# Optimization experiments

Hardware: AMD Instinct MI355X
Metric: run time of the kernel (lower is better)

## Reference

```python
import jax, jax.numpy as jnp
import numpy as np
import math

B = 512          # graphs per batch
NP = 200         # nodes per graph
E_PER = 2000     # edges per graph
V = 50000        # item vocab
EMB = 9
HID = 128
RATIO = 0.8
K1 = math.ceil(RATIO * NP)   # 160
K2 = math.ceil(RATIO * K1)   # 128
K3 = math.ceil(RATIO * K2)   # 103


def sage_conv(x, src, dst, valid, n, w_neigh, w_root, b):
    # PyG SAGEConv: lin_l(mean_{j->i} x_j) + lin_r(x_i) + bias
    msg = x[src] * valid[:, None]                      # [E, C]
    seg = jnp.where(valid > 0, dst, n)                 # invalid edges -> dummy segment
    s = jax.ops.segment_sum(msg, seg, num_segments=n + 1)[:n]
    cnt = jax.ops.segment_sum(valid, seg, num_segments=n + 1)[:n]
    mean = s / jnp.maximum(cnt, 1.0)[:, None]
    return mean @ w_neigh.T + x @ w_root.T + b


def topk_pool(x, src, dst, valid, np_cur, k, p):
    # TopKPooling: score = tanh(x.p/||p||); keep top-k per graph; x *= score
    n = x.shape[0]
    score = jnp.tanh((x @ p) / jnp.linalg.norm(p))
    topv, topi = jax.lax.top_k(score.reshape(B, np_cur), k)   # [B, k]
    kept = (jnp.arange(B)[:, None] * np_cur + topi).reshape(-1)
    n_new = B * k
    x_new = x[kept] * topv.reshape(-1)[:, None]
    mapping = jnp.full((n,), -1, dtype=jnp.int32).at[kept].set(
        jnp.arange(n_new, dtype=jnp.int32))
    ns, nd = mapping[src], mapping[dst]
    valid_new = valid * ((ns >= 0) & (nd >= 0)).astype(valid.dtype)
    return x_new, jnp.maximum(ns, 0), jnp.maximum(nd, 0), valid_new


def global_pool(x, k):
    # cat([global_max_pool, global_mean_pool]) with uniform graph size k
    xr = x.reshape(B, k, -1)
    return jnp.concatenate([xr.max(axis=1), xr.mean(axis=1)], axis=1)


def setup_inputs() -> dict:
    key = jax.random.key(0)
    ks = jax.random.split(key, 24)
    # block-structured intra-graph edges
    s = jax.random.randint(ks[0], (B, E_PER), 0, NP)
    d = jax.random.randint(ks[1], (B, E_PER), 0, NP)
    off = (jnp.arange(B) * NP)[:, None]
    edge_index = jnp.stack([(s + off).reshape(-1), (d + off).reshape(-1)]).astype(jnp.int32)
    node_ids = jax.random.randint(ks[2], (B * NP, 1), 0, V)
    batch = jnp.repeat(jnp.arange(B), NP)
    sc = 0.1
    p = {
        'emb': jax.random.normal(ks[3], (V, EMB)) * sc,
        'w1n': jax.random.normal(ks[4], (HID, EMB)) * sc,
        'w1r': jax.random.normal(ks[5], (HID, EMB)) * sc,
        'b1': jnp.zeros((HID,)),
        'w2n': jax.random.normal(ks[6], (HID, HID)) * sc,
        'w2r': jax.random.normal(ks[7], (HID, HID)) * sc,
        'b2': jnp.zeros((HID,)),
        'w3n': jax.random.normal(ks[8], (HID, HID)) * sc,
        'w3r': jax.random.normal(ks[9], (HID, HID)) * sc,
        'b3': jnp.zeros((HID,)),
        'p1': jax.random.normal(ks[10], (HID,)) * sc,
        'p2': jax.random.normal(ks[11], (HID,)) * sc,
        'p3': jax.random.normal(ks[12], (HID,)) * sc,
        'lw1': jax.random.normal(ks[13], (HID, 2 * HID)) * sc,
        'lb1': jnp.zeros((HID,)),
        'lw2': jax.random.normal(ks[14], (64, HID)) * sc,
        'lb2': jnp.zeros((64,)),
        'lw3': jax.random.normal(ks[15], (1, 64)) * sc,
        'lb3': jnp.zeros((1,)),
    }
    return {'node_ids': node_ids, 'edge_index': edge_index, 'batch': batch, **p}


def reference(node_ids, edge_index, batch, emb, w1n, w1r, b1, w2n, w2r, b2,
              w3n, w3r, b3, p1, p2, p3, lw1, lb1, lw2, lb2, lw3, lb3):
    src, dst = edge_index[0], edge_index[1]
    valid = jnp.ones(src.shape[0], dtype=jnp.float32)
    x = emb[node_ids[:, 0]]                                  # [N, 9]
    x = jax.nn.relu(sage_conv(x, src, dst, valid, B * NP, w1n, w1r, b1))
    x, src, dst, valid = topk_pool(x, src, dst, valid, NP, K1, p1)
    x1 = global_pool(x, K1)
    x = jax.nn.relu(sage_conv(x, src, dst, valid, B * K1, w2n, w2r, b2))
    x, src, dst, valid = topk_pool(x, src, dst, valid, K1, K2, p2)
    x2 = global_pool(x, K2)
    x = jax.nn.relu(sage_conv(x, src, dst, valid, B * K2, w3n, w3r, b3))
    x, src, dst, valid = topk_pool(x, src, dst, valid, K2, K3, p3)
    x3 = global_pool(x, K3)
    h = x1 + x2 + x3                                         # [B, 256]
    h = jax.nn.relu(h @ lw1.T + lb1)
    h = jax.nn.relu(h @ lw2.T + lb2)
    return jax.nn.sigmoid(h @ lw3.T + lb3)[:, 0]             # [B]
```

## Files before the change

### kernel.cpp

```cpp
#include <hip/hip_runtime.h>
#include <math.h>

constexpr int B    = 512;
constexpr int NPG  = 200;
constexpr int EPER = 2000;
constexpr int EMB  = 9;
constexpr int HID  = 128;
constexpr int K1   = 160;
constexpr int K2   = 128;
constexpr int K3   = 103;
constexpr int E    = B * EPER;

__global__ __launch_bounds__(640, 2) void k_fused(
        const int* __restrict__ node_ids,
        const float* __restrict__ emb,
        const int* __restrict__ es, const int* __restrict__ ed,
        const float* __restrict__ w1n, const float* __restrict__ w1r,
        const float* __restrict__ b1, const float* __restrict__ p1,
        const float* __restrict__ w2n, const float* __restrict__ w2r,
        const float* __restrict__ b2, const float* __restrict__ p2,
        const float* __restrict__ w3n, const float* __restrict__ w3r,
        const float* __restrict__ b3, const float* __restrict__ p3,
        float* __restrict__ g1, float* __restrict__ g2,
        float* __restrict__ g3) {
    const int g = blockIdx.x, tid = threadIdx.x;
    const int lane = tid & 63, wv = tid >> 6;

    __shared__ float xY[K1 * 132];
    __shared__ float S[2 * 32 * 132];
    __shared__ int   csr[EPER];
    __shared__ int   deg[256], scanb[256], off2[257], cur[256];
    __shared__ int   idsL[NPG];
    __shared__ float sc[NPG];
    __shared__ int   pos1[NPG], pos2[K1];

    const int eb = g * EPER, nb0 = g * NPG;

    {
        float* x0L  = S;
        float* mnL  = S + 1800;
        float* redA = S + 3600;
        if (tid < NPG) idsL[tid] = node_ids[g * NPG + tid];
        if (tid < 256) deg[tid] = 0;
        __syncthreads();
        for (int i = tid; i < NPG * EMB; i += 640) {
            int n = i / EMB, j = i - n * EMB;
            x0L[i] = emb[(size_t)idsL[n] * EMB + j];
        }
        for (int e = tid; e < EPER; e += 640)
            atomicAdd(&deg[ed[eb + e] - nb0], 1);
        __syncthreads();
        if (tid < 256) scanb[tid] = deg[tid];
        __syncthreads();
        #pragma unroll
        for (int d = 1; d < 256; d <<= 1) {
            int t = (tid < 256 && tid >= d) ? scanb[tid - d] : 0;
            __syncthreads();
            if (tid < 256) scanb[tid] += t;
            __syncthreads();
        }
        if (tid == 0) off2[0] = 0;
        if (tid < 256) off2[tid + 1] = scanb[tid];
        __syncthreads();
        if (tid < 256) cur[tid] = off2[tid];
        __syncthreads();
        for (int e = tid; e < EPER; e += 640) {
            int slot = atomicAdd(&cur[ed[eb + e] - nb0], 1);
            csr[slot] = es[eb + e] - nb0;
        }
        __syncthreads();
        if (tid < NPG) {
            int bg = off2[tid], en = off2[tid + 1];
            float a[EMB];
            #pragma unroll
            for (int j = 0; j < EMB; j++) a[j] = 0.f;
            for (int t = bg; t < en; t++) {
                int s = csr[t];
                #pragma unroll
                for (int j = 0; j < EMB; j++) a[j] += x0L[s * EMB + j];
            }
            float inv = 1.f / (float)((en - bg) > 1 ? (en - bg) : 1);
            #pragma unroll
            for (int j = 0; j < EMB; j++) mnL[tid * EMB + j] = a[j] * inv;
        }
        float pl0 = p1[lane], pl1 = p1[64 + lane];
        float pp = pl0 * pl0 + pl1 * pl1;
        #pragma unroll
        for (int o = 32; o >= 1; o >>= 1) pp += __shfl_xor(pp, o, 64);
        float nrm = sqrtf(pp);
        float wn0[EMB], wn1[EMB], wr0[EMB], wr1[EMB];
        #pragma unroll
        for (int j = 0; j < EMB; j++) {
            wn0[j] = w1n[lane * EMB + j];
            wn1[j] = w1n[(lane + 64) * EMB + j];
            wr0[j] = w1r[lane * EMB + j];
            wr1[j] = w1r[(lane + 64) * EMB + j];
        }
        float bb0 = b1[lane], bb1 = b1[64 + lane];
        __syncthreads();
        for (int i = wv; i < NPG; i += 10) {
            float c0 = bb0, c1 = bb1;
            #pragma unroll
            for (int j = 0; j < EMB; j++) {
                float m = mnL[i * EMB + j];
                float x = x0L[i * EMB + j];
                c0 += m * wn0[j] + x * wr0[j];
                c1 += m * wn1[j] + x * wr1[j];
            }
            c0 = fmaxf(c0, 0.f);
            c1 = fmaxf(c1, 0.f);
            float d = c0 * pl0 + c1 * pl1;
            #pragma unroll
            for (int o = 32; o >= 1; o >>= 1) d += __shfl_xor(d, o, 64);
            if (lane == 0) sc[i] = tanhf(d / nrm);
        }
        __syncthreads();
        if (tid < NPG) {
            float scv = sc[tid];
            int rank = 0;
            for (int j = 0; j < NPG; j++) {
                float o = sc[j];
                rank += (o > scv) || (o == scv && j < tid);
            }
            pos1[tid] = (rank < K1) ? rank : -1;
        }
        __syncthreads();
        float pm0 = -INFINITY, pm1 = -INFINITY, ps0 = 0.f, ps1 = 0.f;
        for (int i = wv; i < NPG; i += 10) {
            int r = pos1[i];
            if (r < 0) continue;
            float c0 = bb0, c1 = bb1;
            #pragma unroll
            for (int j = 0; j < EMB; j++) {
                float m = mnL[i * EMB + j];
                float x = x0L[i * EMB + j];
                c0 += m * wn0[j] + x * wr0[j];
                c1 += m * wn1[j] + x * wr1[j];
            }
            float s = sc[i];
            float v0 = fmaxf(c0, 0.f) * s;
            float v1 = fmaxf(c1, 0.f) * s;
            xY[r * 132 + lane] = v0;
            xY[r * 132 + 64 + lane] = v1;
            pm0 = fmaxf(pm0, v0); ps0 += v0;
            pm1 = fmaxf(pm1, v1); ps1 += v1;
        }
        redA[wv * 128 + lane] = pm0;
        redA[wv * 128 + 64 + lane] = pm1;
        redA[1280 + wv * 128 + lane] = ps0;
        redA[1280 + wv * 128 + 64 + lane] = ps1;
        __syncthreads();
        if (tid < 128) {
            float mx = redA[tid], sm = redA[1280 + tid];
            #pragma unroll
            for (int w = 1; w < 10; w++) {
                mx = fmaxf(mx, redA[w * 128 + tid]);
                sm += redA[1280 + w * 128 + tid];
            }
            g1[g * 256 + tid] = mx;
            g1[g * 256 + 128 + tid] = sm / (float)K1;
        }
        __syncthreads();
    }

    {
        if (tid < 256) deg[tid] = 0;
        __syncthreads();
        for (int e = tid; e < EPER; e += 640) {
            int a = pos1[es[eb + e] - nb0];
            int b = pos1[ed[eb + e] - nb0];
            if (a >= 0 && b >= 0) atomicAdd(&deg[b], 1);
        }
        __syncthreads();
        if (tid < 256) scanb[tid] = deg[tid];
        __syncthreads();
        #pragma unroll
        for (int d = 1; d < 256; d <<= 1) {
            int t = (tid < 256 && tid >= d) ? scanb[tid - d] : 0;
            __syncthreads();
            if (tid < 256) scanb[tid] += t;
            __syncthreads();
        }
        if (tid == 0) off2[0] = 0;
        if (tid < 256) off2[tid + 1] = scanb[tid];
        __syncthreads();
        if (tid < 256) cur[tid] = off2[tid];
        __syncthreads();
        for (int e = tid; e < EPER; e += 640) {
            int a = pos1[es[eb + e] - nb0];
            int b = pos1[ed[eb + e] - nb0];
            if (a >= 0 && b >= 0) {
                int slot = atomicAdd(&cur[b], 1);
                csr[slot] = a;
            }
        }
        __syncthreads();

        const int tc = tid & 31, tr = tid >> 5;
        float accY[8][4], accZ[8][4];
        #pragma unroll
        for (int r = 0; r < 8; r++)
            #pragma unroll
            for (int c = 0; c < 4; c++) { accY[r][c] = 0.f; accZ[r][c] = 0.f; }

        const int sr = tid >> 3, sc4 = (tid & 7) * 4;
        const bool stager = (sr < 64);
        const float* wsrc0 = (sr < 32) ? w2n : w2r;
        const int wrow = (sr < 32) ? sr : sr - 32;
        float* Bmine = S + ((sr < 32) ? 0 : 32 * 132);
        float4 bvv[4];
        if (stager) {
            #pragma unroll
            for (int i = 0; i < 4; i++)
                bvv[i] = *(const float4*)(wsrc0 + (size_t)(wrow + i * 32) * HID + sc4);
        }
        for (int ch = 0; ch < 4; ch++) {
            if (stager) {
                #pragma unroll
                for (int i = 0; i < 4; i++) {
                    int r = wrow + i * 32;
                    Bmine[(sc4 + 0) * 132 + r] = bvv[i].x;
                    Bmine[(sc4 + 1) * 132 + r] = bvv[i].y;
                    Bmine[(sc4 + 2) * 132 + r] = bvv[i].z;
                    Bmine[(sc4 + 3) * 132 + r] = bvv[i].w;
                }
            }
            __syncthreads();
            if (ch + 1 < 4 && stager) {
                #pragma unroll
                for (int i = 0; i < 4; i++)
                    bvv[i] = *(const float4*)(wsrc0 + (size_t)(wrow + i * 32) * HID
                                              + (ch + 1) * 32 + sc4);
            }
            for (int kq = 0; kq < 8; kq++) {
                float4 af[8];
                #pragma unroll
                for (int rr = 0; rr < 8; rr++)
                    af[rr] = *(const float4*)&xY[(tr * 8 + rr) * 132 + ch * 32 + kq * 4];
                #pragma unroll
                for (int kk = 0; kk < 4; kk++) {
                    int k = kq * 4 + kk;
                    float4 bn = *(const float4*)&S[k * 132 + tc * 4];
                    float4 br = *(const float4*)&S[32 * 132 + k * 132 + tc * 4];
                    #pragma unroll
                    for (int rr = 0; rr < 8; rr++) {
                        float a = (kk == 0) ? af[rr].x : (kk == 1) ? af[rr].y
                                 : (kk == 2) ? af[rr].z : af[rr].w;
                        accY[rr][0] += a * bn.x; accY[rr][1] += a * bn.y;
                        accY[rr][2] += a * bn.z; accY[rr][3] += a * bn.w;
                        accZ[rr][0] += a * br.x; accZ[rr][1] += a * br.y;
                        accZ[rr][2] += a * br.z; accZ[rr][3] += a * br.w;
                    }
                }
            }
            __syncthreads();
        }
        #pragma unroll
        for (int rr = 0; rr < 8; rr++) {
            float4 yv = {accY[rr][0], accY[rr][1], accY[rr][2], accY[rr][3]};
            *(float4*)&xY[(tr * 8 + rr) * 132 + tc * 4] = yv;
        }
        __syncthreads();

        float bias[4], pv[4];
        #pragma unroll
        for (int c = 0; c < 4; c++) {
            bias[c] = b2[tc * 4 + c];
            pv[c]   = p2[tc * 4 + c];
        }
        float a0 = p2[lane], a1 = p2[64 + lane];
        float pp = a0 * a0 + a1 * a1;
        #pragma unroll
        for (int o = 32; o >= 1; o >>= 1) pp += __shfl_xor(pp, o, 64);
        float nrm = sqrtf(pp);
        float outv[8][4];
        #pragma unroll
        for (int rr = 0; rr < 8; rr++) {
            int m = tr * 8 + rr;
            int bg = off2[m], en = off2[m + 1];
            float s0 = 0.f, s1 = 0.f, s2 = 0.f, s3 = 0.f;
            for (int t = bg; t < en; t++) {
                float4 yv = *(const float4*)&xY[csr[t] * 132 + tc * 4];
                s0 += yv.x; s1 += yv.y; s2 += yv.z; s3 += yv.w;
            }
            float inv = 1.f / (float)((en - bg) > 1 ? (en - bg) : 1);
            outv[rr][0] = fmaxf(s0 * inv + accZ[rr][0] + bias[0], 0.f);
            outv[rr][1] = fmaxf(s1 * inv + accZ[rr][1] + bias[1], 0.f);
            outv[rr][2] = fmaxf(s2 * inv + accZ[rr][2] + bias[2], 0.f);
            outv[rr][3] = fmaxf(s3 * inv + accZ[rr][3] + bias[3], 0.f);
        }
        float* scpart = S;
        __syncthreads();
        #pragma unroll
        for (int rr = 0; rr < 8; rr++) {
            float sp = outv[rr][0] * pv[0] + outv[rr][1] * pv[1]
                     + outv[rr][2] * pv[2] + outv[rr][3] * pv[3];
            scpart[(tr * 8 + rr) * 32 + tc] = sp;
        }
        __syncthreads();
        if (tid < K1) {
            float sum = 0.f;
            #pragma unroll
            for (int t = 0; t < 32; t++) sum += scpart[tid * 32 + t];
            sc[tid] = tanhf(sum / nrm);
        }
        __syncthreads();
        if (tid < K1) {
            float scv = sc[tid];
            int rank = 0;
            for (int j = 0; j < K1; j++) {
                float o = sc[j];
                rank += (o > scv) || (o == scv && j < tid);
            }
            pos2[tid] = (rank < K2) ? rank : -1;
        }
        __syncthreads();
        float cm[4], cs[4];
        #pragma unroll
        for (int c = 0; c < 4; c++) { cm[c] = -INFINITY; cs[c] = 0.f; }
        #pragma unroll
        for (int rr = 0; rr < 8; rr++) {
            int m = tr * 8 + rr;
            int r = pos2[m];
            if (r < 0) continue;
            float sv = sc[m];
            float v0 = outv[rr][0] * sv, v1 = outv[rr][1] * sv;
            float v2 = outv[rr][2] * sv, v3 = outv[rr][3] * sv;
            cm[0] = fmaxf(cm[0], v0); cs[0] += v0;
            cm[1] = fmaxf(cm[1], v1); cs[1] += v1;
            cm[2] = fmaxf(cm[2], v2); cs[2] += v2;
            cm[3] = fmaxf(cm[3], v3); cs[3] += v3;
            float4 o0 = {v0, v1, v2, v3};
            *(float4*)&xY[r * 132 + tc * 4] = o0;
        }
        float* redM = S;
        float* redS = S + 20 * 128;
        #pragma unroll
        for (int c = 0; c < 4; c++) {
            redM[tr * 128 + tc * 4 + c] = cm[c];
            redS[tr * 128 + tc * 4 + c] = cs[c];
        }
        __syncthreads();
        if (tid < 128) {
            float mx = redM[tid], sm = redS[tid];
            #pragma unroll 4
            for (int t = 1; t < 20; t++) {
                mx = fmaxf(mx, redM[t * 128 + tid]);
                sm += redS[t * 128 + tid];
            }
            g2[g * 256 + tid] = mx;
            g2[g * 256 + 128 + tid] = sm / (float)K2;
        }
        __syncthreads();
    }

    {
        if (tid < 256) deg[tid] = 0;
        __syncthreads();
        for (int e = tid; e < EPER; e += 640) {
            int a = pos1[es[eb + e] - nb0];
            int b = pos1[ed[eb + e] - nb0];
            a = (a >= 0) ? pos2[a] : -1;
            b = (b >= 0) ? pos2[b] : -1;
            if (a >= 0 && b >= 0) atomicAdd(&deg[b], 1);
        }
        __syncthreads();
        if (tid < 256) scanb[tid] = deg[tid];
        __syncthreads();
        #pragma unroll
        for (int d = 1; d < 256; d <<= 1) {
            int t = (tid < 256 && tid >= d) ? scanb[tid - d] : 0;
            __syncthreads();
            if (tid < 256) scanb[tid] += t;
            __syncthreads();
        }
        if (tid == 0) off2[0] = 0;
        if (tid < 256) off2[tid + 1] = scanb[tid];
        __syncthreads();
        if (tid < 256) cur[tid] = off2[tid];
        __syncthreads();
        for (int e = tid; e < EPER; e += 640) {
            int a = pos1[es[eb + e] - nb0];
            int b = pos1[ed[eb + e] - nb0];
            a = (a >= 0) ? pos2[a] : -1;
            b = (b >= 0) ? pos2[b] : -1;
            if (a >= 0 && b >= 0) {
                int slot = atomicAdd(&cur[b], 1);
                csr[slot] = a;
            }
        }
        __syncthreads();

        const int tc = tid & 31, tr = tid >> 5;
        const bool comp = (tid < 512);
        float accY[8][4], accZ[8][4];
        #pragma unroll
        for (int r = 0; r < 8; r++)
            #pragma unroll
            for (int c = 0; c < 4; c++) { accY[r][c] = 0.f; accZ[r][c] = 0.f; }

        const int sr = tid >> 3, sc4 = (tid & 7) * 4;
        const bool stager = (sr < 64);
        const float* wsrc0 = (sr < 32) ? w3n : w3r;
        const int wrow = (sr < 32) ? sr : sr - 32;
        float* Bmine = S + ((sr < 32) ? 0 : 32 * 132);
        float4 bvv[4];
        if (stager) {
            #pragma unroll
            for (int i = 0; i < 4; i++)
                bvv[i] = *(const float4*)(wsrc0 + (size_t)(wrow + i * 32) * HID + sc4);
        }
        for (int ch = 0; ch < 4; ch++) {
            if (stager) {
                #pragma unroll
                for (int i = 0; i < 4; i++) {
                    int r = wrow + i * 32;
                    Bmine[(sc4 + 0) * 132 + r] = bvv[i].x;
                    Bmine[(sc4 + 1) * 132 + r] = bvv[i].y;
                    Bmine[(sc4 + 2) * 132 + r] = bvv[i].z;
                    Bmine[(sc4 + 3) * 132 + r] = bvv[i].w;
                }
            }
            __syncthreads();
            if (ch + 1 < 4 && stager) {
                #pragma unroll
                for (int i = 0; i < 4; i++)
                    bvv[i] = *(const float4*)(wsrc0 + (size_t)(wrow + i * 32) * HID
                                              + (ch + 1) * 32 + sc4);
            }
            if (comp) {
                for (int kq = 0; kq < 8; kq++) {
                    float4 af[8];
                    #pragma unroll
                    for (int rr = 0; rr < 8; rr++)
                        af[rr] = *(const float4*)&xY[(tr * 8 + rr) * 132 + ch * 32 + kq * 4];
                    #pragma unroll
                    for (int kk = 0; kk < 4; kk++) {
                        int k = kq * 4 + kk;
                        float4 bn = *(const float4*)&S[k * 132 + tc * 4];
                        float4 br = *(const float4*)&S[32 * 132 + k * 132 + tc * 4];
                        #pragma unroll
                        for (int rr = 0; rr < 8; rr++) {
                            float a = (kk == 0) ? af[rr].x : (kk == 1) ? af[rr].y
                                     : (kk == 2) ? af[rr].z : af[rr].w;
                            accY[rr][0] += a * bn.x; accY[rr][1] += a * bn.y;
                            accY[rr][2] += a * bn.z; accY[rr][3] += a * bn.w;
                            accZ[rr][0] += a * br.x; accZ[rr][1] += a * br.y;
                            accZ[rr][2] += a * br.z; accZ[rr][3] += a * br.w;
                        }
                    }
                }
            }
            __syncthreads();
        }
        if (comp) {
            #pragma unroll
            for (int rr = 0; rr < 8; rr++) {
                float4 yv = {accY[rr][0], accY[rr][1], accY[rr][2], accY[rr][3]};
                *(float4*)&xY[(tr * 8 + rr) * 132 + tc * 4] = yv;
            }
        }
        __syncthreads();

        float bias[4], pv[4];
        #pragma unroll
        for (int c = 0; c < 4; c++) {
            bias[c] = b3[tc * 4 + c];
            pv[c]   = p3[tc * 4 + c];
        }
        float a0 = p3[lane], a1 = p3[64 + lane];
        float pp = a0 * a0 + a1 * a1;
        #pragma unroll
        for (int o = 32; o >= 1; o >>= 1) pp += __shfl_xor(pp, o, 64);
        float nrm = sqrtf(pp);
        float outv[8][4];
        float* scpart = S;
        if (comp) {
            #pragma unroll
            for (int rr = 0; rr < 8; rr++) {
                int m = tr * 8 + rr;
                int bg = off2[m], en = off2[m + 1];
                float s0 = 0.f, s1 = 0.f, s2 = 0.f, s3 = 0.f;
                for (int t = bg; t < en; t++) {
                    float4 yv = *(const float4*)&xY[csr[t] * 132 + tc * 4];
                    s0 += yv.x; s1 += yv.y; s2 += yv.z; s3 += yv.w;
                }
                float inv = 1.f / (float)((en - bg) > 1 ? (en - bg) : 1);
                outv[rr][0] = fmaxf(s0 * inv + accZ[rr][0] + bias[0], 0.f);
                outv[rr][1] = fmaxf(s1 * inv + accZ[rr][1] + bias[1], 0.f);
                outv[rr][2] = fmaxf(s2 * inv + accZ[rr][2] + bias[2], 0.f);
                outv[rr][3] = fmaxf(s3 * inv + accZ[rr][3] + bias[3], 0.f);
            }
        }
        __syncthreads();
        if (comp) {
            #pragma unroll
            for (int rr = 0; rr < 8; rr++) {
                float sp = outv[rr][0] * pv[0] + outv[rr][1] * pv[1]
                         + outv[rr][2] * pv[2] + outv[rr][3] * pv[3];
                scpart[(tr * 8 + rr) * 32 + tc] = sp;
            }
        }
        __syncthreads();
        if (tid < K2) {
            float sum = 0.f;
            #pragma unroll
            for (int t = 0; t < 32; t++) sum += scpart[tid * 32 + t];
            sc[tid] = tanhf(sum / nrm);
        }
        __syncthreads();
        int* posC = idsL;
        if (tid < K2) {
            float scv = sc[tid];
            int rank = 0;
            for (int j = 0; j < K2; j++) {
                float o = sc[j];
                rank += (o > scv) || (o == scv && j < tid);
            }
            posC[tid] = (rank < K3) ? rank : -1;
        }
        __syncthreads();
        float cm[4], cs[4];
        #pragma unroll
        for (int c = 0; c < 4; c++) { cm[c] = -INFINITY; cs[c] = 0.f; }
        if (comp) {
            #pragma unroll
            for (int rr = 0; rr < 8; rr++) {
                int m = tr * 8 + rr;
                int r = posC[m];
                if (r < 0) continue;
                float sv = sc[m];
                #pragma unroll
                for (int c = 0; c < 4; c++) {
                    float v = outv[rr][c] * sv;
                    cm[c] = fmaxf(cm[c], v);
                    cs[c] += v;
                }
            }
        }
        float* redM = S;
        float* redS = S + 16 * 128;
        if (comp) {
            #pragma unroll
            for (int c = 0; c < 4; c++) {
                redM[tr * 128 + tc * 4 + c] = cm[c];
                redS[tr * 128 + tc * 4 + c] = cs[c];
            }
        }
        __syncthreads();
        if (tid < 128) {
            float mx = redM[tid], sm = redS[tid];
            #pragma unroll 4
            for (int t = 1; t < 16; t++) {
                mx = fmaxf(mx, redM[t * 128 + tid]);
                sm += redS[t * 128 + tid];
            }
            g3[g * 256 + tid] = mx;
            g3[g * 256 + 128 + tid] = sm / (float)K3;
        }
    }
}

__global__ __launch_bounds__(128) void k_mlp(const float* __restrict__ g1, const float* __restrict__ g2,
                      const float* __restrict__ g3,
                      const float* __restrict__ lw1, const float* __restrict__ lb1,
                      const float* __restrict__ lw2, const float* __restrict__ lb2,
                      const float* __restrict__ lw3, const float* __restrict__ lb3,
                      float* __restrict__ out) {
    int g = blockIdx.x, t = threadIdx.x;
    __shared__ float h0[256];
    __shared__ float h1[128];
    __shared__ float h2r[64];
    h0[t]       = g1[g * 256 + t] + g2[g * 256 + t] + g3[g * 256 + t];
    h0[t + 128] = g1[g * 256 + 128 + t] + g2[g * 256 + 128 + t] + g3[g * 256 + 128 + t];
    __syncthreads();
    float a = lb1[t];
    #pragma unroll 4
    for (int j = 0; j < 256; j++) a += h0[j] * lw1[t * 256 + j];
    h1[t] = fmaxf(a, 0.f);
    __syncthreads();
    if (t < 64) {
        float a2 = lb2[t];
        #pragma unroll 4
        for (int j = 0; j < 128; j++) a2 += h1[j] * lw2[t * 128 + j];
        h2r[t] = fmaxf(a2, 0.f) * lw3[t];
    }
    __syncthreads();
    if (t == 0) {
        float s = 0.f;
        for (int j = 0; j < 64; j++) s += h2r[j];
        s += lb3[0];
        out[g] = 1.f / (1.f + expf(-s));
    }
}

extern "C" void kernel_launch(void* const* d_in, const int* in_sizes, int n_in,
                              void* d_out, int out_size, void* d_ws, size_t ws_size,
                              hipStream_t stream) {
    const int*   node_ids = (const int*)d_in[0];
    const int*   ei   = (const int*)d_in[1];
    const float* emb  = (const float*)d_in[3];
    const float* w1n  = (const float*)d_in[4];
    const float* w1r  = (const float*)d_in[5];
    const float* b1   = (const float*)d_in[6];
    const float* w2n  = (const float*)d_in[7];
    const float* w2r  = (const float*)d_in[8];
    const float* b2   = (const float*)d_in[9];
    const float* w3n  = (const float*)d_in[10];
    const float* w3r  = (const float*)d_in[11];
    const float* b3   = (const float*)d_in[12];
    const float* p1   = (const float*)d_in[13];
    const float* p2   = (const float*)d_in[14];
    const float* p3   = (const float*)d_in[15];
    const float* lw1  = (const float*)d_in[16];
    const float* lb1  = (const float*)d_in[17];
    const float* lw2  = (const float*)d_in[18];
    const float* lb2  = (const float*)d_in[19];
    const float* lw3  = (const float*)d_in[20];
    const float* lb3  = (const float*)d_in[21];
    float* out = (float*)d_out;

    float* ws  = (float*)d_ws;
    float* g1  = ws;
    float* g2  = g1 + B * 2 * HID;
    float* g3  = g2 + B * 2 * HID;

    k_fused<<<B, 640, 0, stream>>>(node_ids, emb, ei, ei + E,
                                   w1n, w1r, b1, p1,
                                   w2n, w2r, b2, p2,
                                   w3n, w3r, b3, p3,
                                   g1, g2, g3);
    k_mlp<<<B, 128, 0, stream>>>(g1, g2, g3, lw1, lb1, lw2, lb2, lw3, lb3, out);
}
```

Before: 364.3 us.

## Use wave-shuffle scan for CSR offsets and spill pooled rows to LDS

Replaces the barrier-heavy Hillis-Steele block scan over 256 degree counters with a single-wavefront shuffle scan, removing about 16 block-wide barriers per layer. It also stages the conv outputs in shared memory instead of keeping them live in registers across the top-k ranking. The next layer then gathers its input rows through an inverse permutation (inv2), so pooled rows are not compacted. This cuts register pressure and barriers, at the cost of an extra LDS write/read pass, an indirect row index in the GEMM loads, and a few added syncs.

```diff
diff --git a/kernel.cpp b/kernel.cpp
--- a/kernel.cpp
+++ b/kernel.cpp
@@ -10,6 +10,27 @@
 constexpr int K2   = 128;
 constexpr int K3   = 103;
 constexpr int E    = B * EPER;
+
+__device__ __forceinline__ void scan_off(const int* deg, int* off2,
+                                         int lane, int wv) {
+    if (wv == 0) {
+        int i0 = lane * 4;
+        int v0 = deg[i0], v1 = deg[i0 + 1], v2 = deg[i0 + 2], v3 = deg[i0 + 3];
+        int s1 = v0 + v1, s2 = s1 + v2, s3 = s2 + v3;
+        int run = s3;
+        #pragma unroll
+        for (int o = 1; o < 64; o <<= 1) {
+            int t = __shfl_up(run, o, 64);
+            if (lane >= o) run += t;
+        }
+        int excl = run - s3;
+        off2[i0]     = excl;
+        off2[i0 + 1] = excl + v0;
+        off2[i0 + 2] = excl + s1;
+        off2[i0 + 3] = excl + s2;
+        if (lane == 63) off2[256] = run;
+    }
+}
 
 __global__ __launch_bounds__(640, 2) void k_fused(
         const int* __restrict__ node_ids,
@@ -29,10 +50,10 @@
     __shared__ float xY[K1 * 132];
     __shared__ float S[2 * 32 * 132];
     __shared__ int   csr[EPER];
-    __shared__ int   deg[256], scanb[256], off2[257], cur[256];
+    __shared__ int   deg[256], off2[257], cur[256];
     __shared__ int   idsL[NPG];
     __shared__ float sc[NPG];
-    __shared__ int   pos1[NPG], pos2[K1];
+    __shared__ int   pos1[NPG], pos2[K1], inv2[K2];
 
     const int eb = g * EPER, nb0 = g * NPG;
 
@@ -50,17 +71,7 @@
         for (int e = tid; e < EPER; e += 640)
             atomicAdd(&deg[ed[eb + e] - nb0], 1);
         __syncthreads();
-        if (tid < 256) scanb[tid] = deg[tid];
-        __syncthreads();
-        #pragma unroll
-        for (int d = 1; d < 256; d <<= 1) {
-            int t = (tid < 256 && tid >= d) ? scanb[tid - d] : 0;
-            __syncthreads();
-            if (tid < 256) scanb[tid] += t;
-            __syncthreads();
-        }
-        if (tid == 0) off2[0] = 0;
-        if (tid < 256) off2[tid + 1] = scanb[tid];
+        scan_off(deg, off2, lane, wv);
         __syncthreads();
         if (tid < 256) cur[tid] = off2[tid];
         __syncthreads();
@@ -172,17 +183,7 @@
             if (a >= 0 && b >= 0) atomicAdd(&deg[b], 1);
         }
         __syncthreads();
-        if (tid < 256) scanb[tid] = deg[tid];
-        __syncthreads();
-        #pragma unroll
-        for (int d = 1; d < 256; d <<= 1) {
-            int t = (tid < 256 && tid >= d) ? scanb[tid - d] : 0;
-            __syncthreads();
-            if (tid < 256) scanb[tid] += t;
-            __syncthreads();
-        }
-        if (tid == 0) off2[0] = 0;
-        if (tid < 256) off2[tid + 1] = scanb[tid];
+        scan_off(deg, off2, lane, wv);
         __syncthreads();
         if (tid < 256) cur[tid] = off2[tid];
         __syncthreads();
@@ -290,12 +291,17 @@
             outv[rr][3] = fmaxf(s3 * inv + accZ[rr][3] + bias[3], 0.f);
         }
         float* scpart = S;
-        __syncthreads();
         #pragma unroll
         for (int rr = 0; rr < 8; rr++) {
             float sp = outv[rr][0] * pv[0] + outv[rr][1] * pv[1]
                      + outv[rr][2] * pv[2] + outv[rr][3] * pv[3];
             scpart[(tr * 8 + rr) * 32 + tc] = sp;
+        }
+        __syncthreads();
+        #pragma unroll
+        for (int rr = 0; rr < 8; rr++) {
+            float4 ov = {outv[rr][0], outv[rr][1], outv[rr][2], outv[rr][3]};
+            *(float4*)&xY[(tr * 8 + rr) * 132 + tc * 4] = ov;
         }
         __syncthreads();
         if (tid < K1) {
@@ -313,6 +319,7 @@
                 rank += (o > scv) || (o == scv && j < tid);
             }
             pos2[tid] = (rank < K2) ? rank : -1;
+            if (rank < K2) inv2[rank] = tid;
         }
         __syncthreads();
         float cm[4], cs[4];
@@ -324,15 +331,15 @@
             int r = pos2[m];
             if (r < 0) continue;
             float sv = sc[m];
-            float v0 = outv[rr][0] * sv, v1 = outv[rr][1] * sv;
-            float v2 = outv[rr][2] * sv, v3 = outv[rr][3] * sv;
-            cm[0] = fmaxf(cm[0], v0); cs[0] += v0;
-            cm[1] = fmaxf(cm[1], v1); cs[1] += v1;
-            cm[2] = fmaxf(cm[2], v2); cs[2] += v2;
-            cm[3] = fmaxf(cm[3], v3); cs[3] += v3;
-            float4 o0 = {v0, v1, v2, v3};
-            *(float4*)&xY[r * 132 + tc * 4] = o0;
-        }
+            float4 ov = *(const float4*)&xY[m * 132 + tc * 4];
+            ov.x *= sv; ov.y *= sv; ov.z *= sv; ov.w *= sv;
+            *(float4*)&xY[m * 132 + tc * 4] = ov;
+            cm[0] = fmaxf(cm[0], ov.x); cs[0] += ov.x;
+            cm[1] = fmaxf(cm[1], ov.y); cs[1] += ov.y;
+            cm[2] = fmaxf(cm[2], ov.z); cs[2] += ov.z;
+            cm[3] = fmaxf(cm[3], ov.w); cs[3] += ov.w;
+        }
+        __syncthreads();
         float* redM = S;
         float* redS = S + 20 * 128;
         #pragma unroll
@@ -365,17 +372,7 @@
             if (a >= 0 && b >= 0) atomicAdd(&deg[b], 1);
         }
         __syncthreads();
-        if (tid < 256) scanb[tid] = deg[tid];
-        __syncthreads();
-        #pragma unroll
-        for (int d = 1; d < 256; d <<= 1) {
-            int t = (tid < 256 && tid >= d) ? scanb[tid - d] : 0;
-            __syncthreads();
-            if (tid < 256) scanb[tid] += t;
-            __syncthreads();
-        }
-        if (tid == 0) off2[0] = 0;
-        if (tid < 256) off2[tid + 1] = scanb[tid];
+        scan_off(deg, off2, lane, wv);
         __syncthreads();
         if (tid < 256) cur[tid] = off2[tid];
         __syncthreads();
@@ -393,6 +390,11 @@
 
         const int tc = tid & 31, tr = tid >> 5;
         const bool comp = (tid < 512);
+        int srcrow[8];
+        if (comp) {
+            #pragma unroll
+            for (int rr = 0; rr < 8; rr++) srcrow[rr] = inv2[tr * 8 + rr];
+        }
         float accY[8][4], accZ[8][4];
         #pragma unroll
         for (int r = 0; r < 8; r++)
@@ -433,7 +435,7 @@
                     float4 af[8];
                     #pragma unroll
                     for (int rr = 0; rr < 8; rr++)
-                        af[rr] = *(const float4*)&xY[(tr * 8 + rr) * 132 + ch * 32 + kq * 4];
+                        af[rr] = *(const float4*)&xY[srcrow[rr] * 132 + ch * 32 + kq * 4];
                     #pragma unroll
                     for (int kk = 0; kk < 4; kk++) {
                         int k = kq * 4 + kk;
@@ -491,14 +493,19 @@
                 outv[rr][2] = fmaxf(s2 * inv + accZ[rr][2] + bias[2], 0.f);
                 outv[rr][3] = fmaxf(s3 * inv + accZ[rr][3] + bias[3], 0.f);
             }
-        }
-        __syncthreads();
-        if (comp) {
             #pragma unroll
             for (int rr = 0; rr < 8; rr++) {
                 float sp = outv[rr][0] * pv[0] + outv[rr][1] * pv[1]
                          + outv[rr][2] * pv[2] + outv[rr][3] * pv[3];
                 scpart[(tr * 8 + rr) * 32 + tc] = sp;
+            }
+        }
+        __syncthreads();
+        if (comp) {
+            #pragma unroll
+            for (int rr = 0; rr < 8; rr++) {
+                float4 ov = {outv[rr][0], outv[rr][1], outv[rr][2], outv[rr][3]};
+                *(float4*)&xY[(tr * 8 + rr) * 132 + tc * 4] = ov;
             }
         }
         __syncthreads();
@@ -530,14 +537,14 @@
                 int r = posC[m];
                 if (r < 0) continue;
                 float sv = sc[m];
-                #pragma unroll
-                for (int c = 0; c < 4; c++) {
-                    float v = outv[rr][c] * sv;
-                    cm[c] = fmaxf(cm[c], v);
-                    cs[c] += v;
-                }
-            }
-        }
+                float4 ov = *(const float4*)&xY[m * 132 + tc * 4];
+                cm[0] = fmaxf(cm[0], ov.x * sv); cs[0] += ov.x * sv;
+                cm[1] = fmaxf(cm[1], ov.y * sv); cs[1] += ov.y * sv;
+                cm[2] = fmaxf(cm[2], ov.z * sv); cs[2] += ov.z * sv;
+                cm[3] = fmaxf(cm[3], ov.w * sv); cs[3] += ov.w * sv;
+            }
+        }
+        __syncthreads();
         float* redM = S;
         float* redS = S + 16 * 128;
         if (comp) {
```

Measured after the change: 369.2 us. No clear change (+1.3%).
